# Kernel tuning notes

Hardware: AMD Instinct MI355X
Metric: run time of the kernel (lower is better)

The kernel has to match this reference:

```python
import jax, jax.numpy as jnp
import numpy as np

N_USERS = 100000
N_ITEMS = 50000
N_NODES = N_USERS + N_ITEMS
EMBED = 64
NNZ = 4000000
BATCH = 4096
N_LAYERS = 3


def setup_inputs() -> dict:
    key = jax.random.key(0)
    k = jax.random.split(key, 8)
    return {
        "batch_user": jax.random.randint(k[0], (BATCH,), 0, N_USERS),
        "batch_pos_item": jax.random.randint(k[1], (BATCH,), 0, N_ITEMS),
        "batch_neg_item": jax.random.randint(k[2], (BATCH,), 0, N_ITEMS),
        "embed_user": jax.random.normal(k[3], (N_USERS, EMBED), dtype=jnp.float32) * 0.1,
        "embed_item": jax.random.normal(k[4], (N_ITEMS, EMBED), dtype=jnp.float32) * 0.1,
        "row_idx": jax.random.randint(k[5], (NNZ,), 0, N_NODES),
        "col_idx": jax.random.randint(k[6], (NNZ,), 0, N_NODES),
        "a_vals": jax.random.uniform(k[7], (NNZ,), dtype=jnp.float32),
    }


def reference(batch_user, batch_pos_item, batch_neg_item,
              embed_user, embed_item, row_idx, col_idx, a_vals):
    # E: [N_NODES, D] stacked user+item embeddings
    E = jnp.concatenate([embed_user, embed_item], axis=0)
    acc = E
    for _ in range(N_LAYERS):
        # SpMM in COO form: out[r] += a[e] * E[c[e]]
        msgs = a_vals[:, None] * E[col_idx]            # [NNZ, D]
        E = jax.ops.segment_sum(msgs, row_idx, num_segments=N_NODES)
        acc = acc + E
    out = acc / (N_LAYERS + 1)
    user_g = out[:N_USERS]
    item_g = out[N_USERS:]
    return (user_g[batch_user], item_g[batch_pos_item], item_g[batch_neg_item])
```

## Files before the change

### kernel.cpp

```cpp
#include <hip/hip_runtime.h>

#define N_USERS 100000
#define N_ITEMS 50000
#define N_NODES 150000
#define EMBED   64
#define NNZV    4000000
#define BATCH   4096
#define NBKT    293
#define CAP     16128

__global__ __launch_bounds__(512) void k_parta(
        const int* __restrict__ row, const int* __restrict__ col,
        const float* __restrict__ vals, int* __restrict__ bcnt,
        unsigned long long* __restrict__ staging, int nnz) {
    __shared__ int cnt[512];
    __shared__ int base_s[512];
    int tid = threadIdx.x;
    cnt[tid] = 0;
    __syncthreads();
    int tile0 = blockIdx.x * 16384;
    for (int k = 0; k < 32; k++) {
        int e = tile0 + k * 512 + tid;
        if (e < nnz) atomicAdd(&cnt[row[e] >> 9], 1);
    }
    __syncthreads();
    int c_ = cnt[tid];
    base_s[tid] = c_ ? (tid * CAP + atomicAdd(&bcnt[tid], c_)) : 0;
    __syncthreads();
    cnt[tid] = 0;
    __syncthreads();
    for (int k = 0; k < 32; k++) {
        int e = tile0 + k * 512 + tid;
        if (e < nnz) {
            int r = row[e];
            int b = r >> 9;
            int rank = atomicAdd(&cnt[b], 1);
            unsigned int key = ((unsigned int)(r & 511) << 18) | (unsigned int)col[e];
            unsigned long long rec = (unsigned long long)key
                                   | ((unsigned long long)__float_as_uint(vals[e]) << 32);
            staging[base_s[b] + rank] = rec;
        }
    }
}

__global__ __launch_bounds__(512) void k_partb(
        const int* __restrict__ bcnt,
        const unsigned long long* __restrict__ staging,
        int* __restrict__ row_ptr,
        unsigned long long* __restrict__ edges) {
    __shared__ int s[512];
    __shared__ int cnt[512];
    __shared__ int cur[512];
    __shared__ int base_sh;
    int b = blockIdx.x;
    int t = threadIdx.x;

    int v = (t < NBKT) ? bcnt[t] : 0;
    s[t] = v;
    __syncthreads();
    for (int off = 1; off < 512; off <<= 1) {
        int u = (t >= off) ? s[t - off] : 0;
        __syncthreads();
        s[t] += u;
        __syncthreads();
    }
    if (t == b) base_sh = s[t] - v;
    if (b == 0 && t == 0) row_ptr[N_NODES] = NNZV;
    __syncthreads();
    int base = base_sh;
    int n    = bcnt[b];
    const unsigned long long* sb = staging + (size_t)b * CAP;

    cnt[t] = 0;
    __syncthreads();
    for (int i = t; i < n; i += 512)
        atomicAdd(&cnt[(unsigned int)sb[i] >> 18], 1);
    __syncthreads();
    int c = cnt[t];
    s[t] = c;
    __syncthreads();
    for (int off = 1; off < 512; off <<= 1) {
        int u = (t >= off) ? s[t - off] : 0;
        __syncthreads();
        s[t] += u;
        __syncthreads();
    }
    int excl = s[t] - c;
    cur[t] = excl;
    int r = (b << 9) + t;
    if (r < N_NODES) row_ptr[r] = base + excl;
    __syncthreads();
    for (int i = t; i < n; i += 512) {
        unsigned long long rec = sb[i];
        unsigned int key = (unsigned int)rec;
        int rank = atomicAdd(&cur[key >> 18], 1);
        edges[base + rank] = (rec & 0xFFFFFFFF00000000ull) | (key & 0x3FFFFu);
    }
}

__device__ __forceinline__ float4 spmm_row(const int* row_ptr,
                                           const unsigned long long* edges,
                                           const float4* __restrict__ eu4,
                                           const float4* __restrict__ ei4s,
                                           int r, int lane) {
    int g = lane >> 4;
    int d = lane & 15;
    int start = row_ptr[r];
    int end   = row_ptr[r + 1];
    float4 acc = make_float4(0.f, 0.f, 0.f, 0.f);
    for (int e0 = start; e0 < end; e0 += 64) {
        int ei = e0 + lane;
        unsigned long long rec = 0ull;
        if (ei < end) rec = __builtin_nontemporal_load(edges + ei);
        int clo = (int)(rec & 0xffffffffull);
        int vhi = (int)(rec >> 32);
        int nleft = end - e0;
        int kmax = (nleft + 3) >> 2;
        #pragma unroll 4
        for (int k = 0; k < kmax; k++) {
            int src = 4 * k + g;
            int cc = __shfl(clo, src);
            float vv = __int_as_float(__shfl(vhi, src));
            const float4* basep = (cc < N_USERS) ? eu4 : ei4s;
            float4 e = basep[cc * 16 + d];
            acc.x += vv * e.x;
            acc.y += vv * e.y;
            acc.z += vv * e.z;
            acc.w += vv * e.w;
        }
    }
    acc.x += __shfl_xor(acc.x, 16);
    acc.y += __shfl_xor(acc.y, 16);
    acc.z += __shfl_xor(acc.z, 16);
    acc.w += __shfl_xor(acc.w, 16);
    acc.x += __shfl_xor(acc.x, 32);
    acc.y += __shfl_xor(acc.y, 32);
    acc.z += __shfl_xor(acc.z, 32);
    acc.w += __shfl_xor(acc.w, 32);
    return acc;
}

__global__ void k_spmm4(const int* __restrict__ row_ptr,
                        const unsigned long long* __restrict__ edges,
                        const float4* __restrict__ eu4,
                        const float4* __restrict__ ei4s,
                        float4* __restrict__ Eout) {
    int lane = threadIdx.x & 63;
    int wv   = threadIdx.x >> 6;
    int rbase = (blockIdx.x * 4 + wv) * 4;
    if (rbase >= N_NODES) return;
    int g = lane >> 4;
    int d = lane & 15;
    int st[4], en[4], len[4];
    #pragma unroll
    for (int i = 0; i < 4; i++) {
        int r = rbase + i;
        if (r < N_NODES) { st[i] = row_ptr[r]; en[i] = row_ptr[r + 1]; }
        else             { st[i] = 0;          en[i] = 0; }
        len[i] = en[i] - st[i];
    }
    int maxlen = len[0];
    #pragma unroll
    for (int i = 1; i < 4; i++) maxlen = (len[i] > maxlen) ? len[i] : maxlen;

    float4 acc[4];
    #pragma unroll
    for (int i = 0; i < 4; i++) acc[i] = make_float4(0.f, 0.f, 0.f, 0.f);

    for (int off = 0; off < maxlen; off += 64) {
        int clo[4], vhi[4], kmax[4];
        #pragma unroll
        for (int i = 0; i < 4; i++) {
            int ei = st[i] + off + lane;
            unsigned long long rec = 0ull;
            if (ei < en[i]) rec = __builtin_nontemporal_load(edges + ei);
            clo[i] = (int)(rec & 0xffffffffull);
            vhi[i] = (int)(rec >> 32);
            int nleft = len[i] - off;
            if (nleft < 0) nleft = 0; else if (nleft > 64) nleft = 64;
            kmax[i] = (nleft + 3) >> 2;
        }
        int kmx = (maxlen - off + 3) >> 2; if (kmx > 16) kmx = 16;
        #pragma unroll 4
        for (int k = 0; k < kmx; k++) {
            int src = 4 * k + g;
            #pragma unroll
            for (int i = 0; i < 4; i++) {
                if (k < kmax[i]) {
                    int cc = __shfl(clo[i], src);
                    float vv = __int_as_float(__shfl(vhi[i], src));
                    const float4* bp = (cc < N_USERS) ? eu4 : ei4s;
                    float4 e = bp[cc * 16 + d];
                    acc[i].x += vv * e.x;
                    acc[i].y += vv * e.y;
                    acc[i].z += vv * e.z;
                    acc[i].w += vv * e.w;
                }
            }
        }
    }
    #pragma unroll
    for (int i = 0; i < 4; i++) {
        acc[i].x += __shfl_xor(acc[i].x, 16);
        acc[i].y += __shfl_xor(acc[i].y, 16);
        acc[i].z += __shfl_xor(acc[i].z, 16);
        acc[i].w += __shfl_xor(acc[i].w, 16);
        acc[i].x += __shfl_xor(acc[i].x, 32);
        acc[i].y += __shfl_xor(acc[i].y, 32);
        acc[i].z += __shfl_xor(acc[i].z, 32);
        acc[i].w += __shfl_xor(acc[i].w, 32);
    }
    if (lane < 16) {
        #pragma unroll
        for (int i = 0; i < 4; i++)
            if (rbase + i < N_NODES) Eout[(rbase + i) * 16 + lane] = acc[i];
    }
}

__global__ void k_spmm_batch(const int* __restrict__ row_ptr,
                             const unsigned long long* __restrict__ edges,
                             const float4* __restrict__ Ein,
                             const int* __restrict__ bu, const int* __restrict__ bp,
                             const int* __restrict__ bn,
                             float4* __restrict__ out) {
    int lane = threadIdx.x & 63;
    int j = blockIdx.x * 4 + (threadIdx.x >> 6);
    if (j >= 3 * BATCH) return;
    int r;
    if (j < BATCH)          r = bu[j];
    else if (j < 2 * BATCH) r = N_USERS + bp[j - BATCH];
    else                    r = N_USERS + bn[j - 2 * BATCH];
    float4 acc = spmm_row(row_ptr, edges, Ein, Ein, r, lane);
    if (lane < 16) {
        float4 e2 = Ein[r * 16 + lane];
        float4 o  = out[j * 16 + lane];
        o.x += 0.25f * (acc.x + e2.x);
        o.y += 0.25f * (acc.y + e2.y);
        o.z += 0.25f * (acc.z + e2.z);
        o.w += 0.25f * (acc.w + e2.w);
        out[j * 16 + lane] = o;
    }
}

__global__ void k_gather_init(const int* __restrict__ bu, const int* __restrict__ bp,
                              const int* __restrict__ bn,
                              const float4* __restrict__ eu4,
                              const float4* __restrict__ ei4s,
                              float4* __restrict__ out) {
    int idx = blockIdx.x * blockDim.x + threadIdx.x;
    if (idx >= 3 * BATCH * 16) return;
    int j = idx >> 4;
    int d = idx & 15;
    int node;
    if (j < BATCH)          node = bu[j];
    else if (j < 2 * BATCH) node = N_USERS + bp[j - BATCH];
    else                    node = N_USERS + bn[j - 2 * BATCH];
    const float4* basep = (node < N_USERS) ? eu4 : ei4s;
    float4 v = basep[node * 16 + d];
    v.x *= 0.25f; v.y *= 0.25f; v.z *= 0.25f; v.w *= 0.25f;
    out[idx] = v;
}

__global__ void k_gather_acc(const int* __restrict__ bu, const int* __restrict__ bp,
                             const int* __restrict__ bn, const float4* __restrict__ E,
                             float4* __restrict__ out) {
    int idx = blockIdx.x * blockDim.x + threadIdx.x;
    if (idx >= 3 * BATCH * 16) return;
    int j = idx >> 4;
    int d = idx & 15;
    int node;
    if (j < BATCH)          node = bu[j];
    else if (j < 2 * BATCH) node = N_USERS + bp[j - BATCH];
    else                    node = N_USERS + bn[j - 2 * BATCH];
    float4 v = E[node * 16 + d];
    float4 o = out[idx];
    o.x += 0.25f * v.x; o.y += 0.25f * v.y; o.z += 0.25f * v.z; o.w += 0.25f * v.w;
    out[idx] = o;
}

extern "C" void kernel_launch(void* const* d_in, const int* in_sizes, int n_in,
                              void* d_out, int out_size, void* d_ws, size_t ws_size,
                              hipStream_t stream) {
    const int*   bu   = (const int*)d_in[0];
    const int*   bp   = (const int*)d_in[1];
    const int*   bn   = (const int*)d_in[2];
    const float* eu   = (const float*)d_in[3];
    const float* ei   = (const float*)d_in[4];
    const int*   row  = (const int*)d_in[5];
    const int*   col  = (const int*)d_in[6];
    const float* vals = (const float*)d_in[7];
    float* out = (float*)d_out;

    char* p = (char*)d_ws;
    auto alloc = [&](size_t nbytes) {
        void* r = (void*)p;
        p += (nbytes + 255) & ~(size_t)255;
        return r;
    };
    float*              E_a     = (float*)alloc((size_t)N_NODES * EMBED * 4);
    float*              E_b     = (float*)alloc((size_t)N_NODES * EMBED * 4);
    unsigned long long* edges   = (unsigned long long*)alloc((size_t)NNZV * 8);
    int*                row_ptr = (int*)alloc((N_NODES + 1) * 4);
    int*                bcnt    = (int*)alloc(512 * 4);
    (void)ws_size; (void)n_in; (void)in_sizes; (void)out_size;

    unsigned long long* staging = (unsigned long long*)E_b;

    const float4* eu4  = (const float4*)eu;
    const float4* ei4s = (const float4*)ei - (size_t)N_USERS * 16;

    const int nnz = NNZV;
    hipMemsetAsync(bcnt, 0, 512 * sizeof(int), stream);

    k_parta<<<(nnz + 16383) / 16384, 512, 0, stream>>>(row, col, vals, bcnt, staging, nnz);
    k_partb<<<NBKT, 512, 0, stream>>>(bcnt, staging, row_ptr, edges);

    k_gather_init<<<(3 * BATCH * 16 + 255) / 256, 256, 0, stream>>>(
        bu, bp, bn, eu4, ei4s, (float4*)out);

    k_spmm4<<<(N_NODES + 15) / 16, 256, 0, stream>>>(row_ptr, edges, eu4, ei4s,
                                                     (float4*)E_a);
    k_gather_acc<<<(3 * BATCH * 16 + 255) / 256, 256, 0, stream>>>(
        bu, bp, bn, (const float4*)E_a, (float4*)out);

    k_spmm4<<<(N_NODES + 15) / 16, 256, 0, stream>>>(row_ptr, edges,
                                                     (const float4*)E_a,
                                                     (const float4*)E_a,
                                                     (float4*)E_b);

    k_spmm_batch<<<(3 * BATCH + 3) / 4, 256, 0, stream>>>(
        row_ptr, edges, (const float4*)E_b, bu, bp, bn, (float4*)out);
}
```

Baseline: 518.0 us.

## Build CSR row_ptr via global per-row atomic ranks and multi-kernel scan

Each edge's rank within its row is now taken from a global per-row atomic counter during the first partition pass and stored as a byte beside the staging record. Row pointers come from a three-kernel scan over those row counts. The second pass shrinks to a direct scatter using row_ptr plus the stored rank. This removes the per-bucket LDS histogram, the two block scans and the second staging read from the bucket kernel, at the cost of 4M global atomics, extra launches and an 8-bit rank that assumes no row exceeds 255 edges.

```diff
diff --git a/kernel.cpp b/kernel.cpp
--- a/kernel.cpp
+++ b/kernel.cpp
@@ -8,11 +8,14 @@
 #define BATCH   4096
 #define NBKT    293
 #define CAP     16128
+#define SRB     293
 
 __global__ __launch_bounds__(512) void k_parta(
         const int* __restrict__ row, const int* __restrict__ col,
         const float* __restrict__ vals, int* __restrict__ bcnt,
-        unsigned long long* __restrict__ staging, int nnz) {
+        unsigned int* __restrict__ rowcnt,
+        unsigned long long* __restrict__ staging,
+        unsigned char* __restrict__ staging8, int nnz) {
     __shared__ int cnt[512];
     __shared__ int base_s[512];
     int tid = threadIdx.x;
@@ -35,66 +38,79 @@
             int r = row[e];
             int b = r >> 9;
             int rank = atomicAdd(&cnt[b], 1);
+            int slot = base_s[b] + rank;
+            unsigned int rkr = atomicAdd(&rowcnt[r], 1u);
             unsigned int key = ((unsigned int)(r & 511) << 18) | (unsigned int)col[e];
             unsigned long long rec = (unsigned long long)key
                                    | ((unsigned long long)__float_as_uint(vals[e]) << 32);
-            staging[base_s[b] + rank] = rec;
+            staging[slot]  = rec;
+            staging8[slot] = (unsigned char)rkr;
         }
     }
 }
 
-__global__ __launch_bounds__(512) void k_partb(
+__global__ __launch_bounds__(512) void k_rscanA(const unsigned int* __restrict__ rowcnt,
+                                                int* __restrict__ bsum) {
+    __shared__ int sh[512];
+    int t = threadIdx.x;
+    int i = blockIdx.x * 512 + t;
+    sh[t] = (i < N_NODES) ? (int)rowcnt[i] : 0;
+    __syncthreads();
+    for (int off = 256; off > 0; off >>= 1) {
+        if (t < off) sh[t] += sh[t + off];
+        __syncthreads();
+    }
+    if (t == 0) bsum[blockIdx.x] = sh[0];
+}
+__global__ __launch_bounds__(512) void k_rscanB(int* __restrict__ bsum) {
+    __shared__ int sh[512];
+    int t = threadIdx.x;
+    int v = (t < SRB) ? bsum[t] : 0;
+    sh[t] = v;
+    __syncthreads();
+    for (int off = 1; off < 512; off <<= 1) {
+        int u = (t >= off) ? sh[t - off] : 0;
+        __syncthreads();
+        sh[t] += u;
+        __syncthreads();
+    }
+    if (t < SRB) bsum[t] = sh[t] - v;
+}
+__global__ __launch_bounds__(512) void k_rscanC(const unsigned int* __restrict__ rowcnt,
+                                                const int* __restrict__ bsum,
+                                                int* __restrict__ row_ptr) {
+    __shared__ int sh[512];
+    int t = threadIdx.x;
+    int i = blockIdx.x * 512 + t;
+    int v = (i < N_NODES) ? (int)rowcnt[i] : 0;
+    sh[t] = v;
+    __syncthreads();
+    for (int off = 1; off < 512; off <<= 1) {
+        int u = (t >= off) ? sh[t - off] : 0;
+        __syncthreads();
+        sh[t] += u;
+        __syncthreads();
+    }
+    if (i < N_NODES) row_ptr[i] = bsum[blockIdx.x] + sh[t] - v;
+    if (i == 0) row_ptr[N_NODES] = NNZV;
+}
+
+__global__ __launch_bounds__(512) void k_partb_lite(
         const int* __restrict__ bcnt,
         const unsigned long long* __restrict__ staging,
-        int* __restrict__ row_ptr,
+        const unsigned char* __restrict__ staging8,
+        const int* __restrict__ row_ptr,
         unsigned long long* __restrict__ edges) {
-    __shared__ int s[512];
-    __shared__ int cnt[512];
-    __shared__ int cur[512];
-    __shared__ int base_sh;
     int b = blockIdx.x;
-    int t = threadIdx.x;
-
-    int v = (t < NBKT) ? bcnt[t] : 0;
-    s[t] = v;
-    __syncthreads();
-    for (int off = 1; off < 512; off <<= 1) {
-        int u = (t >= off) ? s[t - off] : 0;
-        __syncthreads();
-        s[t] += u;
-        __syncthreads();
-    }
-    if (t == b) base_sh = s[t] - v;
-    if (b == 0 && t == 0) row_ptr[N_NODES] = NNZV;
-    __syncthreads();
-    int base = base_sh;
-    int n    = bcnt[b];
-    const unsigned long long* sb = staging + (size_t)b * CAP;
-
-    cnt[t] = 0;
-    __syncthreads();
-    for (int i = t; i < n; i += 512)
-        atomicAdd(&cnt[(unsigned int)sb[i] >> 18], 1);
-    __syncthreads();
-    int c = cnt[t];
-    s[t] = c;
-    __syncthreads();
-    for (int off = 1; off < 512; off <<= 1) {
-        int u = (t >= off) ? s[t - off] : 0;
-        __syncthreads();
-        s[t] += u;
-        __syncthreads();
-    }
-    int excl = s[t] - c;
-    cur[t] = excl;
-    int r = (b << 9) + t;
-    if (r < N_NODES) row_ptr[r] = base + excl;
-    __syncthreads();
-    for (int i = t; i < n; i += 512) {
+    int n = bcnt[b];
+    const unsigned long long* sb = staging  + (size_t)b * CAP;
+    const unsigned char*      s8 = staging8 + (size_t)b * CAP;
+    for (int i = threadIdx.x; i < n; i += 512) {
         unsigned long long rec = sb[i];
         unsigned int key = (unsigned int)rec;
-        int rank = atomicAdd(&cur[key >> 18], 1);
-        edges[base + rank] = (rec & 0xFFFFFFFF00000000ull) | (key & 0x3FFFFu);
+        int r = (b << 9) + (int)(key >> 18);
+        int dst = row_ptr[r] + (int)s8[i];
+        edges[dst] = (rec & 0xFFFFFFFF00000000ull) | (key & 0x3FFFFu);
     }
 }
 
@@ -301,19 +317,27 @@
     float*              E_b     = (float*)alloc((size_t)N_NODES * EMBED * 4);
     unsigned long long* edges   = (unsigned long long*)alloc((size_t)NNZV * 8);
     int*                row_ptr = (int*)alloc((N_NODES + 1) * 4);
+    unsigned int*       rowcnt  = (unsigned int*)alloc((size_t)N_NODES * 4);
     int*                bcnt    = (int*)alloc(512 * 4);
+    int*                bsum    = (int*)alloc((size_t)SRB * 4);
     (void)ws_size; (void)n_in; (void)in_sizes; (void)out_size;
 
-    unsigned long long* staging = (unsigned long long*)E_b;
+    unsigned long long* staging  = (unsigned long long*)E_b;
+    unsigned char*      staging8 = (unsigned char*)E_a;
 
     const float4* eu4  = (const float4*)eu;
     const float4* ei4s = (const float4*)ei - (size_t)N_USERS * 16;
 
     const int nnz = NNZV;
     hipMemsetAsync(bcnt, 0, 512 * sizeof(int), stream);
-
-    k_parta<<<(nnz + 16383) / 16384, 512, 0, stream>>>(row, col, vals, bcnt, staging, nnz);
-    k_partb<<<NBKT, 512, 0, stream>>>(bcnt, staging, row_ptr, edges);
+    hipMemsetAsync(rowcnt, 0, (size_t)N_NODES * 4, stream);
+
+    k_parta<<<(nnz + 16383) / 16384, 512, 0, stream>>>(
+        row, col, vals, bcnt, rowcnt, staging, staging8, nnz);
+    k_rscanA<<<SRB, 512, 0, stream>>>(rowcnt, bsum);
+    k_rscanB<<<1, 512, 0, stream>>>(bsum);
+    k_rscanC<<<SRB, 512, 0, stream>>>(rowcnt, bsum, row_ptr);
+    k_partb_lite<<<NBKT, 512, 0, stream>>>(bcnt, staging, staging8, row_ptr, edges);
 
     k_gather_init<<<(3 * BATCH * 16 + 255) / 256, 256, 0, stream>>>(
         bu, bp, bn, eu4, ei4s, (float4*)out);
```

Result: slower. 680.6 us (+31.4%).
